# Performance work log

Hardware: AMD Instinct MI355X
Metric: run time of the kernel (lower is better)

Reference implementation:

```python
import jax, jax.numpy as jnp
import numpy as np

M, N, D, P = 1024, 1024, 64, 4096
H = N // D
L = P + M  # total KV length


def setup_inputs() -> dict:
    key = jax.random.key(0)
    ks = jax.random.split(key, 7)
    s = 1.0 / np.float32(np.sqrt(N))
    return {
        "X": jax.random.normal(ks[0], (M, N), jnp.float32),
        "W_q": jax.random.normal(ks[1], (N, N), jnp.float32) * s,
        "W_k": jax.random.normal(ks[2], (N, N), jnp.float32) * s,
        "W_v": jax.random.normal(ks[3], (N, N), jnp.float32) * s,
        "cache_K": jax.random.normal(ks[4], (H, P, D), jnp.float32),
        "cache_V": jax.random.normal(ks[5], (H, P, D), jnp.float32),
        "noise": jax.random.normal(ks[6], (H, M, L), jnp.float32) * 0.5,
    }


def reference(X, W_q, W_k, W_v, cache_K, cache_V, noise):
    # Projections: [M, N] -> [M, H, D]
    q = (X @ W_q).reshape(M, H, D)
    k = (X @ W_k).reshape(M, H, D).transpose(1, 0, 2)  # [H, M, D]
    v = (X @ W_v).reshape(M, H, D).transpose(1, 0, 2)  # [H, M, D]

    # KV cache concat (HND layout): [H, L, D]
    k_cache = jnp.concatenate([cache_K, k], axis=1)
    v_cache = jnp.concatenate([cache_V, v], axis=1)

    # Full QK^T scores, sm_scale=1.0, non-causal (flashinfer default): [H, M, L]
    scores = jnp.einsum("mhd,hld->hml", q, k_cache)
    weights = jax.nn.softmax(scores, axis=-1)  # == flash-attention probs (sm_scale=1.0)

    # Attention output: [M, H, D] -> [M, N]
    output = jnp.einsum("hml,hld->mhd", weights, v_cache).reshape(M, N)

    # Keyformer noise-perturbed importance softmax (temperature 1.5): [H, M, L]
    perturb_out = jax.nn.softmax((scores + noise) / 1.5, axis=-1)

    return output, weights, perturb_out
```

## Files before the change

### kernel.cpp

```cpp
#include <hip/hip_runtime.h>
#include <stdint.h>

#define MM 1024
#define NN 1024
#define DD 64
#define PP 4096
#define HH 16
#define LL 5120
#define SHC 12.0f

typedef float  f32x4  __attribute__((ext_vector_type(4)));
typedef short  s16x8  __attribute__((ext_vector_type(8)));
typedef short  s16x4  __attribute__((ext_vector_type(4)));
typedef __bf16 bf16x8 __attribute__((ext_vector_type(8)));

static __device__ __forceinline__ unsigned short f2bf(float f) {
    unsigned u = __float_as_uint(f);
    u += 0x7FFFu + ((u >> 16) & 1u);
    return (unsigned short)(u >> 16);
}
static __device__ __forceinline__ float bf2f(unsigned short h) {
    return __uint_as_float(((unsigned)h) << 16);
}
static __device__ __forceinline__ f32x4 mfma16(s16x8 a, s16x8 b, f32x4 c) {
    return __builtin_amdgcn_mfma_f32_16x16x32_bf16(
        __builtin_bit_cast(bf16x8, a), __builtin_bit_cast(bf16x8, b), c, 0, 0, 0);
}

__global__ void k_prep(const float* __restrict__ X, const float* __restrict__ cK,
                       unsigned short* __restrict__ Xh, unsigned short* __restrict__ Xl,
                       unsigned short* __restrict__ Kall) {
    const int nX4 = (MM * NN) / 4;
    const int nK4 = (HH * PP * DD) / 4;
    int stride = gridDim.x * blockDim.x;
    for (int i = blockIdx.x * blockDim.x + threadIdx.x; i < nX4 + nK4; i += stride) {
        if (i < nX4) {
            f32x4 v = reinterpret_cast<const f32x4*>(X)[i];
            s16x4 h, l;
            for (int j = 0; j < 4; ++j) {
                float f = v[j];
                unsigned short hb = f2bf(f);
                h[j] = (short)hb;
                l[j] = (short)f2bf(f - bf2f(hb));
            }
            reinterpret_cast<s16x4*>(Xh)[i] = h;
            reinterpret_cast<s16x4*>(Xl)[i] = l;
        } else {
            int j = i - nX4;
            f32x4 v = reinterpret_cast<const f32x4*>(cK)[j];
            s16x4 h;
            for (int jj = 0; jj < 4; ++jj) h[jj] = (short)f2bf(v[jj]);
            int e = j * 4;
            int hh = e >> 18;
            int rem = e & 262143;
            int64_t de = (int64_t)hh * (LL * DD) + rem;
            *reinterpret_cast<s16x4*>(Kall + de) = h;
        }
    }
}

__global__ void k_transW(const float* __restrict__ Wq, const float* __restrict__ Wk,
                         const float* __restrict__ Wv,
                         unsigned short* __restrict__ WhT, unsigned short* __restrict__ WlT) {
    __shared__ float t[64][68];
    int z = blockIdx.z;
    const float* W = (z == 0) ? Wq : ((z == 1) ? Wk : Wv);
    int n0 = blockIdx.x * 64, k0 = blockIdx.y * 64;
    int tc = threadIdx.x & 15, tr = threadIdx.x >> 4;
    for (int i = 0; i < 4; ++i) {
        int r = tr + i * 16;
        f32x4 v = *reinterpret_cast<const f32x4*>(W + (int64_t)(k0 + r) * NN + n0 + tc * 4);
        t[r][tc * 4 + 0] = v[0]; t[r][tc * 4 + 1] = v[1];
        t[r][tc * 4 + 2] = v[2]; t[r][tc * 4 + 3] = v[3];
    }
    __syncthreads();
    int64_t zoff = (int64_t)z * MM * NN;
    for (int i = 0; i < 4; ++i) {
        int rr = tr + i * 16;
        s16x4 h, l;
        for (int j = 0; j < 4; ++j) {
            float f = t[tc * 4 + j][rr];
            unsigned short hb = f2bf(f);
            h[j] = (short)hb;
            l[j] = (short)f2bf(f - bf2f(hb));
        }
        *reinterpret_cast<s16x4*>(WhT + zoff + (int64_t)(n0 + rr) * NN + k0 + tc * 4) = h;
        *reinterpret_cast<s16x4*>(WlT + zoff + (int64_t)(n0 + rr) * NN + k0 + tc * 4) = l;
    }
}

__launch_bounds__(256, 4)
__global__ void k_gemm(const unsigned short* __restrict__ Xh, const unsigned short* __restrict__ Xl,
                       const unsigned short* __restrict__ WhT, const unsigned short* __restrict__ WlT,
                       unsigned short* __restrict__ Qh, unsigned short* __restrict__ Ql,
                       unsigned short* __restrict__ Kall, unsigned short* __restrict__ Vproj) {
    __shared__ unsigned short sb[2 * 64 * 72];
    unsigned short* As = sb;
    unsigned short* Bs = sb + 64 * 72;
    int z = blockIdx.z;
    int n0 = blockIdx.x * 64, m0 = blockIdx.y * 64;
    int tid = threadIdx.x, lane = tid & 63, wave = tid >> 6;
    int lrow = lane & 15, lgrp = lane >> 4;
    int wm = (wave >> 1) * 32, wn = (wave & 1) * 32;
    f32x4 acc[2][2] = {};
    for (int seg = 0; seg < 3; ++seg) {
        const unsigned short* Asrc = (seg == 2) ? Xl : Xh;
        const unsigned short* Bsrc = ((seg == 1) ? WlT : WhT) + (int64_t)z * MM * NN;
        for (int kt = 0; kt < 16; ++kt) {
            int kb = kt * 64;
            for (int i = 0; i < 2; ++i) {
                int idx = i * 256 + tid;
                int r = idx >> 3, c8 = (idx & 7) * 8;
                *reinterpret_cast<s16x8*>(&As[r * 72 + c8]) =
                    *reinterpret_cast<const s16x8*>(Asrc + (int64_t)(m0 + r) * NN + kb + c8);
                *reinterpret_cast<s16x8*>(&Bs[r * 72 + c8]) =
                    *reinterpret_cast<const s16x8*>(Bsrc + (int64_t)(n0 + r) * NN + kb + c8);
            }
            __syncthreads();
            for (int ks = 0; ks < 2; ++ks) {
                s16x8 af[2], bfr[2];
                for (int f = 0; f < 2; ++f)
                    af[f] = *reinterpret_cast<const s16x8*>(&As[(wm + f * 16 + lrow) * 72 + ks * 32 + lgrp * 8]);
                for (int f = 0; f < 2; ++f)
                    bfr[f] = *reinterpret_cast<const s16x8*>(&Bs[(wn + f * 16 + lrow) * 72 + ks * 32 + lgrp * 8]);
                for (int i = 0; i < 2; ++i)
                    for (int j = 0; j < 2; ++j)
                        acc[i][j] = mfma16(af[i], bfr[j], acc[i][j]);
            }
            __syncthreads();
        }
    }
    unsigned short* Cs = sb;
    auto stageC = [&](int lo) {
        for (int i = 0; i < 2; ++i)
            for (int j = 0; j < 2; ++j)
                for (int r = 0; r < 4; ++r) {
                    float v = acc[i][j][r];
                    unsigned short hv = f2bf(v);
                    if (lo) hv = f2bf(v - bf2f(hv));
                    Cs[(wm + i * 16 + lgrp * 4 + r) * 72 + wn + j * 16 + lrow] = hv;
                }
    };
    auto writeC = [&](unsigned short* dst, int kmode) {
        for (int i = 0; i < 2; ++i) {
            int idx = i * 256 + tid;
            int r = idx >> 3, c8 = (idx & 7) * 8;
            s16x8 v = *reinterpret_cast<const s16x8*>(&Cs[r * 72 + c8]);
            int gm = m0 + r, gn = n0 + c8;
            if (kmode) {
                int hh = gn >> 6, d = gn & 63;
                *reinterpret_cast<s16x8*>(dst + ((int64_t)hh * LL + PP + gm) * DD + d) = v;
            } else {
                *reinterpret_cast<s16x8*>(dst + (int64_t)gm * NN + gn) = v;
            }
        }
    };
    __syncthreads();
    if (z == 0) {
        stageC(0); __syncthreads(); writeC(Qh, 0);
        __syncthreads(); stageC(1); __syncthreads(); writeC(Ql, 0);
    } else if (z == 1) {
        stageC(0); __syncthreads(); writeC(Kall, 1);
    } else {
        stageC(0); __syncthreads(); writeC(Vproj, 0);
    }
}

__global__ void k_transV(const float* __restrict__ cV, const unsigned short* __restrict__ Vproj,
                         unsigned short* __restrict__ VT) {
    __shared__ unsigned short Ts[64][72];
    int b = blockIdx.x;
    int hh = b / 80, lt = b % 80;
    int l0 = lt * 64;
    int tid = threadIdx.x;
    if (l0 < PP) {
        for (int i = 0; i < 4; ++i) {
            int idx = i * 256 + tid;
            int r = idx >> 4, c4 = (idx & 15) * 4;
            f32x4 v = *reinterpret_cast<const f32x4*>(cV + ((int64_t)hh * PP + l0 + r) * DD + c4);
            s16x4 o;
            for (int j = 0; j < 4; ++j) o[j] = (short)f2bf(v[j]);
            *reinterpret_cast<s16x4*>(&Ts[r][c4]) = o;
        }
    } else {
        for (int i = 0; i < 2; ++i) {
            int idx = i * 256 + tid;
            int r = idx >> 3, c8 = (idx & 7) * 8;
            *reinterpret_cast<s16x8*>(&Ts[r][c8]) =
                *reinterpret_cast<const s16x8*>(Vproj + (int64_t)(l0 - PP + r) * NN + hh * DD + c8);
        }
    }
    __syncthreads();
    for (int i = 0; i < 2; ++i) {
        int idx = i * 256 + tid;
        int d = idx >> 3, l8 = (idx & 7) * 8;
        s16x8 v;
        for (int j = 0; j < 8; ++j) v[j] = (short)Ts[l8 + j][d];
        *reinterpret_cast<s16x8*>(VT + ((int64_t)hh * DD + d) * LL + l0 + l8) = v;
    }
}

__launch_bounds__(256, 4)
__global__ void k_attn2(const unsigned short* __restrict__ Qh, const unsigned short* __restrict__ Ql,
                        const unsigned short* __restrict__ Kall, const unsigned short* __restrict__ VT,
                        const float* __restrict__ noise,
                        float* __restrict__ outO, float* __restrict__ outW, float* __restrict__ outP) {
    __shared__ float sc[16][272];
    __shared__ unsigned short wls[16][264];

    int id = blockIdx.x;
    int xcd = id & 7, j = id >> 3;
    int hh = xcd * 2 + (j >> 6);
    int mt = j & 63;
    int m0 = mt * 16;
    int tid = threadIdx.x, lane = tid & 63, wave = tid >> 6;
    int lrow = lane & 15, lgrp = lane >> 4;
    int erow = tid >> 4, cb = tid & 15;

    s16x8 aqh[2], aql[2];
    for (int ks = 0; ks < 2; ++ks) {
        int64_t off = (int64_t)(m0 + lrow) * NN + hh * DD + ks * 32 + lgrp * 8;
        aqh[ks] = *reinterpret_cast<const s16x8*>(Qh + off);
        aql[ks] = *reinterpret_cast<const s16x8*>(Ql + off);
    }
    const unsigned short* Kh = Kall + (int64_t)hh * LL * DD;
    const unsigned short* Vh = VT + (int64_t)hh * DD * LL;
    const float* nzr = noise + ((int64_t)hh * MM + m0 + erow) * LL;
    float* Wr = outW + ((int64_t)hh * MM + m0 + erow) * LL;
    float* Pr = outP + ((int64_t)hh * MM + m0 + erow) * LL;

    float Sw = 0.f, Sp = 0.f;
    for (int c = 0; c < 20; ++c) {
        int c0 = c * 256;
        f32x4 nv[4];
        for (int q = 0; q < 4; ++q)
            nv[q] = *reinterpret_cast<const f32x4*>(nzr + c0 + q * 64 + cb * 4);
        {
            f32x4 sacc[4] = {};
            int lb = c0 + wave * 64;
            for (int ks = 0; ks < 2; ++ks)
                for (int lf = 0; lf < 4; ++lf) {
                    s16x8 bk = *reinterpret_cast<const s16x8*>(
                        Kh + (int64_t)(lb + lf * 16 + lrow) * DD + ks * 32 + lgrp * 8);
                    sacc[lf] = mfma16(aqh[ks], bk, sacc[lf]);
                    sacc[lf] = mfma16(aql[ks], bk, sacc[lf]);
                }
            for (int lf = 0; lf < 4; ++lf)
                for (int r = 0; r < 4; ++r)
                    sc[lgrp * 4 + r][wave * 64 + lf * 16 + lrow] = sacc[lf][r];
        }
        __syncthreads();
        for (int q = 0; q < 4; ++q) {
            int col = q * 64 + cb * 4;
            f32x4 s = *reinterpret_cast<const f32x4*>(&sc[erow][col]);
            for (int jj = 0; jj < 4; ++jj) {
                Sw += __expf(s[jj] - SHC);
                Sp += __expf((s[jj] + nv[q][jj]) * (1.f / 1.5f) - SHC);
            }
        }
        __syncthreads();
    }
    for (int d = 1; d < 16; d <<= 1) {
        Sw += __shfl_xor(Sw, d, 64);
        Sp += __shfl_xor(Sp, d, 64);
    }
    float iw = 1.f / Sw, ip = 1.f / Sp;

    f32x4 oacc[4] = {};
    for (int c = 19; c >= 0; --c) {
        int c0 = c * 256;
        f32x4 nv[4];
        for (int q = 0; q < 4; ++q)
            nv[q] = *reinterpret_cast<const f32x4*>(nzr + c0 + q * 64 + cb * 4);
        {
            f32x4 sacc[4] = {};
            int lb = c0 + wave * 64;
            for (int ks = 0; ks < 2; ++ks)
                for (int lf = 0; lf < 4; ++lf) {
                    s16x8 bk = *reinterpret_cast<const s16x8*>(
                        Kh + (int64_t)(lb + lf * 16 + lrow) * DD + ks * 32 + lgrp * 8);
                    sacc[lf] = mfma16(aqh[ks], bk, sacc[lf]);
                    sacc[lf] = mfma16(aql[ks], bk, sacc[lf]);
                }
            for (int lf = 0; lf < 4; ++lf)
                for (int r = 0; r < 4; ++r)
                    sc[lgrp * 4 + r][wave * 64 + lf * 16 + lrow] = sacc[lf][r];
        }
        __syncthreads();
        for (int q = 0; q < 4; ++q) {
            int col = q * 64 + cb * 4;
            f32x4 s = *reinterpret_cast<const f32x4*>(&sc[erow][col]);
            f32x4 wv, pv;
            for (int jj = 0; jj < 4; ++jj) {
                wv[jj] = __expf(s[jj] - SHC) * iw;
                pv[jj] = __expf((s[jj] + nv[q][jj]) * (1.f / 1.5f) - SHC) * ip;
            }
            *reinterpret_cast<f32x4*>(Wr + c0 + col) = wv;
            *reinterpret_cast<f32x4*>(Pr + c0 + col) = pv;
            s16x4 pk;
            for (int jj = 0; jj < 4; ++jj) pk[jj] = (short)f2bf(wv[jj]);
            *reinterpret_cast<s16x4*>(&wls[erow][col]) = pk;
        }
        __syncthreads();
        for (int ks = 0; ks < 2; ++ks) {
            int k0 = wave * 64 + ks * 32;
            s16x8 bw = *reinterpret_cast<const s16x8*>(&wls[lrow][k0 + lgrp * 8]);
            for (int df = 0; df < 4; ++df) {
                s16x8 av = *reinterpret_cast<const s16x8*>(
                    Vh + (int64_t)(df * 16 + lrow) * LL + c0 + k0 + lgrp * 8);
                oacc[df] = mfma16(av, bw, oacc[df]);
            }
        }
    }
    __syncthreads();
    float* ored = &sc[0][0];
    for (int df = 0; df < 4; ++df)
        for (int r = 0; r < 4; ++r)
            ored[(wave * 64 + df * 16 + lgrp * 4 + r) * 17 + lrow] = oacc[df][r];
    __syncthreads();
    for (int i = 0; i < 4; ++i) {
        int idx = i * 256 + tid;
        int m = idx >> 6, d = idx & 63;
        float v = ored[d * 17 + m] + ored[(64 + d) * 17 + m] +
                  ored[(128 + d) * 17 + m] + ored[(192 + d) * 17 + m];
        outO[(int64_t)(m0 + m) * NN + hh * DD + d] = v;
    }
}

extern "C" void kernel_launch(void* const* d_in, const int* in_sizes, int n_in,
                              void* d_out, int out_size, void* d_ws, size_t ws_size,
                              hipStream_t stream) {
    const float* X  = (const float*)d_in[0];
    const float* Wq = (const float*)d_in[1];
    const float* Wk = (const float*)d_in[2];
    const float* Wv = (const float*)d_in[3];
    const float* cK = (const float*)d_in[4];
    const float* cV = (const float*)d_in[5];
    const float* nz = (const float*)d_in[6];

    char* ws = (char*)d_ws;
    const int64_t U = 1 << 21;
    unsigned short* Xh    = (unsigned short*)(ws + 0 * U);
    unsigned short* Xl    = (unsigned short*)(ws + 1 * U);
    unsigned short* WhT   = (unsigned short*)(ws + 2 * U);
    unsigned short* WlT   = (unsigned short*)(ws + 5 * U);
    unsigned short* Qh    = (unsigned short*)(ws + 8 * U);
    unsigned short* Ql    = (unsigned short*)(ws + 9 * U);
    unsigned short* Kall  = (unsigned short*)(ws + 10 * U);
    unsigned short* Vproj = (unsigned short*)(ws + 15 * U);
    unsigned short* VT    = (unsigned short*)(ws + 16 * U);

    float* outO = (float*)d_out;
    float* outW = outO + (int64_t)MM * NN;
    float* outP = outW + (int64_t)HH * MM * LL;

    k_prep<<<2048, 256, 0, stream>>>(X, cK, Xh, Xl, Kall);
    k_transW<<<dim3(16, 16, 3), 256, 0, stream>>>(Wq, Wk, Wv, WhT, WlT);
    k_gemm<<<dim3(16, 16, 3), 256, 0, stream>>>(Xh, Xl, WhT, WlT, Qh, Ql, Kall, Vproj);
    k_transV<<<1280, 256, 0, stream>>>(cV, Vproj, VT);
    k_attn2<<<1024, 256, 0, stream>>>(Qh, Ql, Kall, VT, nz, outO, outW, outP);
}
```

Measured before the change: 483.5 us.

## Compute softmax row sums in MFMA registers, dropping LDS round trip in pass one

```diff
diff --git a/kernel.cpp b/kernel.cpp
--- a/kernel.cpp
+++ b/kernel.cpp
@@ -205,8 +205,10 @@
                         const unsigned short* __restrict__ Kall, const unsigned short* __restrict__ VT,
                         const float* __restrict__ noise,
                         float* __restrict__ outO, float* __restrict__ outW, float* __restrict__ outP) {
-    __shared__ float sc[16][272];
+    __shared__ float sc[16][276];
     __shared__ unsigned short wls[16][264];
+    __shared__ float sred[4][16][2];
+    __shared__ float siwp[16][2];
 
     int id = blockIdx.x;
     int xcd = id & 7, j = id >> 3;
@@ -225,13 +227,60 @@
     }
     const unsigned short* Kh = Kall + (int64_t)hh * LL * DD;
     const unsigned short* Vh = VT + (int64_t)hh * DD * LL;
-    const float* nzr = noise + ((int64_t)hh * MM + m0 + erow) * LL;
+    const float* nzw = noise + ((int64_t)hh * MM + m0) * LL;
+    const float* nzr = nzw + (int64_t)erow * LL;
     float* Wr = outW + ((int64_t)hh * MM + m0 + erow) * LL;
     float* Pr = outP + ((int64_t)hh * MM + m0 + erow) * LL;
 
-    float Sw = 0.f, Sp = 0.f;
+    float Sw4[4] = {}, Sp4[4] = {};
     for (int c = 0; c < 20; ++c) {
         int c0 = c * 256;
+        int lb = c0 + wave * 64;
+        float nzv[4][4];
+        for (int r = 0; r < 4; ++r)
+            for (int lf = 0; lf < 4; ++lf)
+                nzv[r][lf] = nzw[(int64_t)(lgrp * 4 + r) * LL + lb + lf * 16 + lrow];
+        f32x4 sacc[4] = {};
+        for (int ks = 0; ks < 2; ++ks)
+            for (int lf = 0; lf < 4; ++lf) {
+                s16x8 bk = *reinterpret_cast<const s16x8*>(
+                    Kh + (int64_t)(lb + lf * 16 + lrow) * DD + ks * 32 + lgrp * 8);
+                sacc[lf] = mfma16(aqh[ks], bk, sacc[lf]);
+                sacc[lf] = mfma16(aql[ks], bk, sacc[lf]);
+            }
+        for (int lf = 0; lf < 4; ++lf)
+            for (int r = 0; r < 4; ++r) {
+                float s = sacc[lf][r];
+                Sw4[r] += __expf(s - SHC);
+                Sp4[r] += __expf((s + nzv[r][lf]) * (1.f / 1.5f) - SHC);
+            }
+    }
+    for (int r = 0; r < 4; ++r)
+        for (int d = 1; d < 16; d <<= 1) {
+            Sw4[r] += __shfl_xor(Sw4[r], d, 64);
+            Sp4[r] += __shfl_xor(Sp4[r], d, 64);
+        }
+    if (lrow == 0)
+        for (int r = 0; r < 4; ++r) {
+            sred[wave][lgrp * 4 + r][0] = Sw4[r];
+            sred[wave][lgrp * 4 + r][1] = Sp4[r];
+        }
+    __syncthreads();
+    if (tid < 32) {
+        int row = tid >> 1, ty = tid & 1;
+        float S = sred[0][row][ty] + sred[1][row][ty] + sred[2][row][ty] + sred[3][row][ty];
+        siwp[row][ty] = 1.f / S;
+    }
+    __syncthreads();
+    float iw = siwp[erow][0], ip = siwp[erow][1];
+
+    f32x4 oacc[4] = {};
+    for (int c = 19; c >= 0; --c) {
+        int c0 = c * 256;
+        s16x8 vv[4];
+        for (int df = 0; df < 4; ++df)
+            vv[df] = *reinterpret_cast<const s16x8*>(
+                Vh + (int64_t)(df * 16 + lrow) * LL + c0 + wave * 64 + lgrp * 8);
         f32x4 nv[4];
         for (int q = 0; q < 4; ++q)
             nv[q] = *reinterpret_cast<const f32x4*>(nzr + c0 + q * 64 + cb * 4);
@@ -253,43 +302,6 @@
         for (int q = 0; q < 4; ++q) {
             int col = q * 64 + cb * 4;
             f32x4 s = *reinterpret_cast<const f32x4*>(&sc[erow][col]);
-            for (int jj = 0; jj < 4; ++jj) {
-                Sw += __expf(s[jj] - SHC);
-                Sp += __expf((s[jj] + nv[q][jj]) * (1.f / 1.5f) - SHC);
-            }
-        }
-        __syncthreads();
-    }
-    for (int d = 1; d < 16; d <<= 1) {
-        Sw += __shfl_xor(Sw, d, 64);
-        Sp += __shfl_xor(Sp, d, 64);
-    }
-    float iw = 1.f / Sw, ip = 1.f / Sp;
-
-    f32x4 oacc[4] = {};
-    for (int c = 19; c >= 0; --c) {
-        int c0 = c * 256;
-        f32x4 nv[4];
-        for (int q = 0; q < 4; ++q)
-            nv[q] = *reinterpret_cast<const f32x4*>(nzr + c0 + q * 64 + cb * 4);
-        {
-            f32x4 sacc[4] = {};
-            int lb = c0 + wave * 64;
-            for (int ks = 0; ks < 2; ++ks)
-                for (int lf = 0; lf < 4; ++lf) {
-                    s16x8 bk = *reinterpret_cast<const s16x8*>(
-                        Kh + (int64_t)(lb + lf * 16 + lrow) * DD + ks * 32 + lgrp * 8);
-                    sacc[lf] = mfma16(aqh[ks], bk, sacc[lf]);
-                    sacc[lf] = mfma16(aql[ks], bk, sacc[lf]);
-                }
-            for (int lf = 0; lf < 4; ++lf)
-                for (int r = 0; r < 4; ++r)
-                    sc[lgrp * 4 + r][wave * 64 + lf * 16 + lrow] = sacc[lf][r];
-        }
-        __syncthreads();
-        for (int q = 0; q < 4; ++q) {
-            int col = q * 64 + cb * 4;
-            f32x4 s = *reinterpret_cast<const f32x4*>(&sc[erow][col]);
             f32x4 wv, pv;
             for (int jj = 0; jj < 4; ++jj) {
                 wv[jj] = __expf(s[jj] - SHC) * iw;
@@ -302,13 +314,16 @@
             *reinterpret_cast<s16x4*>(&wls[erow][col]) = pk;
         }
         __syncthreads();
-        for (int ks = 0; ks < 2; ++ks) {
-            int k0 = wave * 64 + ks * 32;
-            s16x8 bw = *reinterpret_cast<const s16x8*>(&wls[lrow][k0 + lgrp * 8]);
+        {
+            int k0 = wave * 64;
+            s16x8 bw0 = *reinterpret_cast<const s16x8*>(&wls[lrow][k0 + lgrp * 8]);
+            for (int df = 0; df < 4; ++df)
+                oacc[df] = mfma16(vv[df], bw0, oacc[df]);
+            s16x8 bw1 = *reinterpret_cast<const s16x8*>(&wls[lrow][k0 + 32 + lgrp * 8]);
             for (int df = 0; df < 4; ++df) {
                 s16x8 av = *reinterpret_cast<const s16x8*>(
-                    Vh + (int64_t)(df * 16 + lrow) * LL + c0 + k0 + lgrp * 8);
-                oacc[df] = mfma16(av, bw, oacc[df]);
+                    Vh + (int64_t)(df * 16 + lrow) * LL + c0 + k0 + 32 + lgrp * 8);
+                oacc[df] = mfma16(av, bw1, oacc[df]);
             }
         }
     }
```

Result: slower. 531.6 us (+10.0%).
